# Kernel tuning notes

Measured on AMD Instinct MI355X. Metric: run time of the kernel, lower is better.

Reference implementation:

```python
import jax, jax.numpy as jnp
import numpy as np

K = 9  # kernel_size (knn neighbors, loop=True -> self included)

def setup_inputs() -> dict:
    key = jax.random.key(0)
    k1, k2, k3 = jax.random.split(key, 3)
    B, C, H, W = 8, 64, 32, 32
    OUT = 64
    x = jax.random.normal(k1, (B, C, H, W), dtype=jnp.float32)
    # SAGEConv params: lin_l (neighbor aggregate, with bias), lin_r (root, no bias)
    s = 1.0 / np.sqrt(C)
    W_l = jax.random.uniform(k2, (OUT, C), minval=-s, maxval=s, dtype=jnp.float32)
    b_l = jnp.zeros((OUT,), dtype=jnp.float32)
    W_r = jax.random.uniform(k3, (OUT, C), minval=-s, maxval=s, dtype=jnp.float32)
    return {"x": x, "W_l": W_l, "b_l": b_l, "W_r": W_r}

def _knn_mean(x_f, batches):
    # squared-euclidean pairwise distances [N, N], masked across batches
    sq = jnp.sum(x_f * x_f, axis=-1)
    dist = sq[:, None] + sq[None, :] - 2.0 * (x_f @ x_f.T)
    cross = batches[:, None] != batches[None, :]
    dist = jnp.where(cross, jnp.inf, dist)
    neg, idx = jax.lax.top_k(-dist, K)          # k nearest (self included, dist 0)
    valid = (neg != -jnp.inf).astype(x_f.dtype)  # handle degenerate last-batch node
    nbr = x_f[idx] * valid[..., None]            # [N, K, C]
    return nbr.sum(axis=1) / valid.sum(axis=1, keepdims=True)

def reference(x, W_l, b_l, W_r):
    B, C, H, Wd = x.shape
    N = B * H * Wd
    x_f = x.transpose(0, 2, 3, 1).reshape(N, C)  # flat_nodes: [B*H*W, C]
    # torch.linspace(0, B, steps=N).to(int64): truncation of i*B/(N-1)
    batches = jnp.linspace(0.0, float(B), N).astype(jnp.int32)
    mean_nbr = _knn_mean(x_f, batches)
    # SAGEConv: lin_l(mean_j x_j) + lin_r(x_i)
    return mean_nbr @ W_l.T + b_l + x_f @ W_r.T
```

## Files before the change

kernel.cpp:

```cpp
#include <hip/hip_runtime.h>
#include <cstdint>
#include <cstddef>


typedef float nf4 __attribute__((ext_vector_type(4)));

__global__ __launch_bounds__(256, 2) void k_all(const float* __restrict__ x,
                                                const float* __restrict__ Wl,
                                                const float* __restrict__ bl,
                                                const float* __restrict__ Wr,
                                                float* __restrict__ out) {
  __shared__ float R0[16384];
  __shared__ float Asf[1024];
  __shared__ float sqX[1024];
  float4* Xs4 = (float4*)R0;
  float4* As4 = (float4*)Asf;
  float4* sqX4 = (float4*)sqX;

  int bi = (int)blockIdx.x, t = threadIdx.x;
  int n0 = bi << 4;
  int s = (n0 >= 7168) ? 7168 : (n0 & ~1023);
  const float* xb = x + (((size_t)(s >> 10)) << 16);
  const float* xrow = x + (((size_t)(n0 >> 10)) << 16) + (n0 & 1023);

  {
    int c = t >> 2, r4 = t & 3;
    As4[(c << 2) + r4] = *(const float4*)&xrow[((size_t)c << 10) + (r4 << 2)];
  }

  float acc[8][8];
#pragma unroll
  for (int r = 0; r < 8; ++r)
#pragma unroll
    for (int c = 0; c < 8; ++c) acc[r][c] = 0.f;
  float4 p4 = {0.f, 0.f, 0.f, 0.f};
  int h = t >> 7, cg = t & 127;

#pragma unroll 1
  for (int ks = 0; ks < 4; ++ks) {
    if (ks) __syncthreads();
    int k0 = ks << 4;
#pragma unroll 4
    for (int i = 0; i < 16; ++i) {
      int lin = t + (i << 8);
      int kc = lin >> 8, j4 = lin & 255;
      Xs4[(kc << 8) + j4] =
          *(const float4*)&xb[((size_t)(k0 + kc) << 10) + (j4 << 2)];
    }
    __syncthreads();
#pragma unroll
    for (int kc = 0; kc < 16; ++kc) {
      float4 v = Xs4[(kc << 8) + t];
      p4.x = fmaf(v.x, v.x, p4.x);
      p4.y = fmaf(v.y, v.y, p4.y);
      p4.z = fmaf(v.z, v.z, p4.z);
      p4.w = fmaf(v.w, v.w, p4.w);
    }
#pragma unroll
    for (int kc = 0; kc < 16; ++kc) {
      float4 a0 = As4[((k0 + kc) << 2) + (h << 1)];
      float4 a1 = As4[((k0 + kc) << 2) + (h << 1) + 1];
      float4 b0 = Xs4[(kc << 8) + cg];
      float4 b1 = Xs4[(kc << 8) + 128 + cg];
      float av[8] = {a0.x, a0.y, a0.z, a0.w, a1.x, a1.y, a1.z, a1.w};
      float bv[8] = {b0.x, b0.y, b0.z, b0.w, b1.x, b1.y, b1.z, b1.w};
#pragma unroll
      for (int r = 0; r < 8; ++r)
#pragma unroll
        for (int c = 0; c < 8; ++c)
          acc[r][c] = fmaf(av[r], bv[c], acc[r][c]);
    }
  }
  sqX4[t] = p4;
  __syncthreads();

  {
    float4 sj0 = sqX4[cg];
    float4 sj1 = sqX4[128 + cg];
    int jb = (n0 - s) + (h << 3);
#pragma unroll
    for (int r = 0; r < 8; ++r) {
      float si = sqX[jb + r];
      nf4 o0 = {si + sj0.x - 2.f * acc[r][0], si + sj0.y - 2.f * acc[r][1],
                si + sj0.z - 2.f * acc[r][2], si + sj0.w - 2.f * acc[r][3]};
      nf4 o1 = {si + sj1.x - 2.f * acc[r][4], si + sj1.y - 2.f * acc[r][5],
                si + sj1.z - 2.f * acc[r][6], si + sj1.w - 2.f * acc[r][7]};
      int row = (h << 3) + r;
      *(nf4*)&R0[(row << 10) + (cg << 2)] = o0;
      *(nf4*)&R0[(row << 10) + 512 + (cg << 2)] = o1;
    }
  }
  __syncthreads();

  int lane = t & 63, w = t >> 6;
  float msum[4], xr[4];
  int cnt[4];
#pragma unroll 1
  for (int rr = 0; rr < 4; ++rr) {
    int rl = (w << 2) + rr;
    int n = n0 + rl;
    float xself = x[(((size_t)(n >> 10)) << 16) + ((size_t)lane << 10) + (n & 1023)];
    xr[rr] = xself;
    if (n == 8191) { msum[rr] = xself; cnt[rr] = 1; continue; }
    cnt[rr] = 9;
    bool mlast = (n >= 7168);
    unsigned long long cand[16];
#pragma unroll
    for (int q = 0; q < 4; ++q) {
      nf4 v = *(const nf4*)&R0[(rl << 10) + (q << 8) + (lane << 2)];
      float vv[4] = {v.x, v.y, v.z, v.w};
#pragma unroll
      for (int e = 0; e < 4; ++e) {
        unsigned u = __float_as_uint(vv[e]);
        u = (u & 0x80000000u) ? ~u : (u | 0x80000000u);
        unsigned jj = (unsigned)((q << 8) + (lane << 2) + e);
        cand[(q << 2) + e] = ((unsigned long long)u << 32) | jj;
      }
    }
    if (mlast && lane == 63) cand[15] = ~0ull;
    unsigned long long m1 = cand[0], m2 = cand[1];
    if (m2 < m1) { unsigned long long tt = m1; m1 = m2; m2 = tt; }
#pragma unroll
    for (int q = 2; q < 16; ++q) {
      unsigned long long c = cand[q];
      unsigned long long lo = (c < m1) ? c : m1;
      unsigned long long hi = (c < m1) ? m1 : c;
      m2 = (hi < m2) ? hi : m2;
      m1 = lo;
    }
    unsigned long long lm = m1;
    unsigned rmask = 0;
    bool stale = false;
    unsigned jloc[9];
#pragma unroll
    for (int kk = 0; kk < 9; ++kk) {
      unsigned long long g = lm;
#pragma unroll
      for (int off = 32; off; off >>= 1) {
        unsigned ghi = __shfl_xor((unsigned)(g >> 32), off, 64);
        unsigned glo = __shfl_xor((unsigned)g, off, 64);
        unsigned long long o = ((unsigned long long)ghi << 32) | glo;
        g = (o < g) ? o : g;
      }
      jloc[kk] = (unsigned)g & 1023u;
      if (lm == g) {
        unsigned slot = (((unsigned)g >> 6) & 12u) | ((unsigned)g & 3u);
        rmask |= 1u << slot;
        if (!stale) { lm = m2; stale = true; }
        else {
          unsigned long long best = ~0ull;
#pragma unroll
          for (int q = 0; q < 16; ++q) {
            bool alive = ((rmask >> q) & 1u) == 0u;
            unsigned long long c = cand[q];
            best = (alive && c < best) ? c : best;
          }
          lm = best;
        }
      }
    }
    const float* gx = xb + ((size_t)lane << 10);
    float g0 = gx[jloc[0]], g1 = gx[jloc[1]], g2 = gx[jloc[2]];
    float g3 = gx[jloc[3]], g4 = gx[jloc[4]], g5 = gx[jloc[5]];
    float g6 = gx[jloc[6]], g7 = gx[jloc[7]], g8 = gx[jloc[8]];
    msum[rr] = (((g0 + g1) + (g2 + g3)) + ((g4 + g5) + (g6 + g7))) + g8;
  }
  __syncthreads();

#pragma unroll 4
  for (int i = 0; i < 16; ++i) {
    int lin = t + (i << 8);
    int o = lin >> 6, c = lin & 63;
    R0[o * 65 + c] = Wl[lin];
    R0[4160 + o * 65 + c] = Wr[lin];
  }
  __syncthreads();

  float bias = bl[lane];
  float ms[4];
#pragma unroll
  for (int rr = 0; rr < 4; ++rr)
    ms[rr] = (cnt[rr] == 9) ? msum[rr] * (1.f / 9.f) : msum[rr];
  float accL[4] = {0.f, 0.f, 0.f, 0.f};
  float accR[4] = {0.f, 0.f, 0.f, 0.f};
#pragma unroll
  for (int c = 0; c < 64; ++c) {
    float wlc = R0[lane * 65 + c];
    float wrc = R0[4160 + lane * 65 + c];
#pragma unroll
    for (int rr = 0; rr < 4; ++rr) {
      float mc = __int_as_float(__builtin_amdgcn_readlane(__float_as_int(ms[rr]), c));
      float xc = __int_as_float(__builtin_amdgcn_readlane(__float_as_int(xr[rr]), c));
      accL[rr] = fmaf(mc, wlc, accL[rr]);
      accR[rr] = fmaf(xc, wrc, accR[rr]);
    }
  }
#pragma unroll
  for (int rr = 0; rr < 4; ++rr)
    __builtin_nontemporal_store(accL[rr] + accR[rr] + bias,
                                &out[((size_t)(n0 + (w << 2) + rr) << 6) + lane]);
}

extern "C" void kernel_launch(void* const* d_in, const int* in_sizes, int n_in,
                              void* d_out, int out_size, void* d_ws, size_t ws_size,
                              hipStream_t stream) {
  const float* x  = (const float*)d_in[0];
  const float* Wl = (const float*)d_in[1];
  const float* bl = (const float*)d_in[2];
  const float* Wr = (const float*)d_in[3];
  float* out = (float*)d_out;
  (void)d_ws; (void)ws_size;

  k_all<<<dim3(512), 256, 0, stream>>>(x, Wl, bl, Wr, out);
}
```

Measured before the change: 104.6 us.

## Halve rows per block and keep distance tiles in registers for top-k

Each block now handles 8 query rows instead of 16, and the grid doubles to 1024 blocks. The GEMM tile is remapped so each wave computes the distances for its own two rows across all 1024 candidates. The top-k selection then reads those distances straight from registers, so the 16x1024 distance buffer in shared memory and its extra barrier are gone. Shared memory per block drops enough to allow 4 blocks per CU. The cost is that the candidate tile of x is loaded and the squared norms are recomputed twice as often across the grid.

```diff
diff --git a/kernel.cpp b/kernel.cpp
--- a/kernel.cpp
+++ b/kernel.cpp
@@ -3,45 +3,44 @@
 #include <cstddef>
 
 
-typedef float nf4 __attribute__((ext_vector_type(4)));
-
-__global__ __launch_bounds__(256, 2) void k_all(const float* __restrict__ x,
+__global__ __launch_bounds__(256, 4) void k_all(const float* __restrict__ x,
                                                 const float* __restrict__ Wl,
                                                 const float* __restrict__ bl,
                                                 const float* __restrict__ Wr,
                                                 float* __restrict__ out) {
-  __shared__ float R0[16384];
-  __shared__ float Asf[1024];
-  __shared__ float sqX[1024];
-  float4* Xs4 = (float4*)R0;
-  float4* As4 = (float4*)Asf;
+  __shared__ float SH[9728];
+  float* Xs = SH;
+  float* Asf = SH + 8192;
+  float* sqX = SH + 8704;
+  float4* Xs4 = (float4*)Xs;
   float4* sqX4 = (float4*)sqX;
 
   int bi = (int)blockIdx.x, t = threadIdx.x;
-  int n0 = bi << 4;
+  int lane = t & 63, w = t >> 6;
+  int n0 = bi << 3;
   int s = (n0 >= 7168) ? 7168 : (n0 & ~1023);
   const float* xb = x + (((size_t)(s >> 10)) << 16);
   const float* xrow = x + (((size_t)(n0 >> 10)) << 16) + (n0 & 1023);
 
-  {
-    int c = t >> 2, r4 = t & 3;
-    As4[(c << 2) + r4] = *(const float4*)&xrow[((size_t)c << 10) + (r4 << 2)];
-  }
-
-  float acc[8][8];
-#pragma unroll
-  for (int r = 0; r < 8; ++r)
-#pragma unroll
-    for (int c = 0; c < 8; ++c) acc[r][c] = 0.f;
+  if (t < 128) {
+    int ch = t >> 1, hf = t & 1;
+    *(float4*)&Asf[(ch << 3) + (hf << 2)] =
+        *(const float4*)&xrow[((size_t)ch << 10) + (hf << 2)];
+  }
+
+  float acc[2][16];
+#pragma unroll
+  for (int r = 0; r < 2; ++r)
+#pragma unroll
+    for (int c = 0; c < 16; ++c) acc[r][c] = 0.f;
   float4 p4 = {0.f, 0.f, 0.f, 0.f};
-  int h = t >> 7, cg = t & 127;
 
 #pragma unroll 1
-  for (int ks = 0; ks < 4; ++ks) {
+  for (int ks = 0; ks < 8; ++ks) {
     if (ks) __syncthreads();
-    int k0 = ks << 4;
-#pragma unroll 4
-    for (int i = 0; i < 16; ++i) {
+    int k0 = ks << 3;
+#pragma unroll
+    for (int i = 0; i < 8; ++i) {
       int lin = t + (i << 8);
       int kc = lin >> 8, j4 = lin & 255;
       Xs4[(kc << 8) + j4] =
@@ -49,7 +48,7 @@
     }
     __syncthreads();
 #pragma unroll
-    for (int kc = 0; kc < 16; ++kc) {
+    for (int kc = 0; kc < 8; ++kc) {
       float4 v = Xs4[(kc << 8) + t];
       p4.x = fmaf(v.x, v.x, p4.x);
       p4.y = fmaf(v.y, v.y, p4.y);
@@ -57,61 +56,47 @@
       p4.w = fmaf(v.w, v.w, p4.w);
     }
 #pragma unroll
-    for (int kc = 0; kc < 16; ++kc) {
-      float4 a0 = As4[((k0 + kc) << 2) + (h << 1)];
-      float4 a1 = As4[((k0 + kc) << 2) + (h << 1) + 1];
-      float4 b0 = Xs4[(kc << 8) + cg];
-      float4 b1 = Xs4[(kc << 8) + 128 + cg];
-      float av[8] = {a0.x, a0.y, a0.z, a0.w, a1.x, a1.y, a1.z, a1.w};
-      float bv[8] = {b0.x, b0.y, b0.z, b0.w, b1.x, b1.y, b1.z, b1.w};
-#pragma unroll
-      for (int r = 0; r < 8; ++r)
-#pragma unroll
-        for (int c = 0; c < 8; ++c)
-          acc[r][c] = fmaf(av[r], bv[c], acc[r][c]);
+    for (int kc = 0; kc < 8; ++kc) {
+      float2 a = *(const float2*)&Asf[((k0 + kc) << 3) + (w << 1)];
+      float4 b0 = Xs4[(kc << 8) + lane];
+      float4 b1 = Xs4[(kc << 8) + 64 + lane];
+      float4 b2 = Xs4[(kc << 8) + 128 + lane];
+      float4 b3 = Xs4[(kc << 8) + 192 + lane];
+      float bv[16] = {b0.x, b0.y, b0.z, b0.w, b1.x, b1.y, b1.z, b1.w,
+                      b2.x, b2.y, b2.z, b2.w, b3.x, b3.y, b3.z, b3.w};
+#pragma unroll
+      for (int c = 0; c < 16; ++c) {
+        acc[0][c] = fmaf(a.x, bv[c], acc[0][c]);
+        acc[1][c] = fmaf(a.y, bv[c], acc[1][c]);
+      }
     }
   }
   sqX4[t] = p4;
   __syncthreads();
 
-  {
-    float4 sj0 = sqX4[cg];
-    float4 sj1 = sqX4[128 + cg];
-    int jb = (n0 - s) + (h << 3);
-#pragma unroll
-    for (int r = 0; r < 8; ++r) {
-      float si = sqX[jb + r];
-      nf4 o0 = {si + sj0.x - 2.f * acc[r][0], si + sj0.y - 2.f * acc[r][1],
-                si + sj0.z - 2.f * acc[r][2], si + sj0.w - 2.f * acc[r][3]};
-      nf4 o1 = {si + sj1.x - 2.f * acc[r][4], si + sj1.y - 2.f * acc[r][5],
-                si + sj1.z - 2.f * acc[r][6], si + sj1.w - 2.f * acc[r][7]};
-      int row = (h << 3) + r;
-      *(nf4*)&R0[(row << 10) + (cg << 2)] = o0;
-      *(nf4*)&R0[(row << 10) + 512 + (cg << 2)] = o1;
-    }
-  }
-  __syncthreads();
-
-  int lane = t & 63, w = t >> 6;
-  float msum[4], xr[4];
-  int cnt[4];
+  float4 sq4[4];
+#pragma unroll
+  for (int q = 0; q < 4; ++q) sq4[q] = sqX4[(q << 6) + lane];
+
+  float msum[2], xr[2];
+  int cnt[2];
 #pragma unroll 1
-  for (int rr = 0; rr < 4; ++rr) {
-    int rl = (w << 2) + rr;
-    int n = n0 + rl;
+  for (int rr = 0; rr < 2; ++rr) {
+    int n = n0 + (w << 1) + rr;
     float xself = x[(((size_t)(n >> 10)) << 16) + ((size_t)lane << 10) + (n & 1023)];
     xr[rr] = xself;
     if (n == 8191) { msum[rr] = xself; cnt[rr] = 1; continue; }
     cnt[rr] = 9;
+    float si = sqX[n - s];
     bool mlast = (n >= 7168);
     unsigned long long cand[16];
 #pragma unroll
     for (int q = 0; q < 4; ++q) {
-      nf4 v = *(const nf4*)&R0[(rl << 10) + (q << 8) + (lane << 2)];
-      float vv[4] = {v.x, v.y, v.z, v.w};
+      float sj[4] = {sq4[q].x, sq4[q].y, sq4[q].z, sq4[q].w};
 #pragma unroll
       for (int e = 0; e < 4; ++e) {
-        unsigned u = __float_as_uint(vv[e]);
+        float d = (si + sj[e]) - 2.f * acc[rr][(q << 2) + e];
+        unsigned u = __float_as_uint(d);
         u = (u & 0x80000000u) ? ~u : (u | 0x80000000u);
         unsigned jj = (unsigned)((q << 8) + (lane << 2) + e);
         cand[(q << 2) + e] = ((unsigned long long)u << 32) | jj;
@@ -167,28 +152,28 @@
   }
   __syncthreads();
 
-#pragma unroll 4
+#pragma unroll
   for (int i = 0; i < 16; ++i) {
     int lin = t + (i << 8);
     int o = lin >> 6, c = lin & 63;
-    R0[o * 65 + c] = Wl[lin];
-    R0[4160 + o * 65 + c] = Wr[lin];
+    SH[o * 65 + c] = Wl[lin];
+    SH[4160 + o * 65 + c] = Wr[lin];
   }
   __syncthreads();
 
   float bias = bl[lane];
-  float ms[4];
-#pragma unroll
-  for (int rr = 0; rr < 4; ++rr)
+  float ms[2];
+#pragma unroll
+  for (int rr = 0; rr < 2; ++rr)
     ms[rr] = (cnt[rr] == 9) ? msum[rr] * (1.f / 9.f) : msum[rr];
-  float accL[4] = {0.f, 0.f, 0.f, 0.f};
-  float accR[4] = {0.f, 0.f, 0.f, 0.f};
+  float accL[2] = {0.f, 0.f};
+  float accR[2] = {0.f, 0.f};
 #pragma unroll
   for (int c = 0; c < 64; ++c) {
-    float wlc = R0[lane * 65 + c];
-    float wrc = R0[4160 + lane * 65 + c];
-#pragma unroll
-    for (int rr = 0; rr < 4; ++rr) {
+    float wlc = SH[lane * 65 + c];
+    float wrc = SH[4160 + lane * 65 + c];
+#pragma unroll
+    for (int rr = 0; rr < 2; ++rr) {
       float mc = __int_as_float(__builtin_amdgcn_readlane(__float_as_int(ms[rr]), c));
       float xc = __int_as_float(__builtin_amdgcn_readlane(__float_as_int(xr[rr]), c));
       accL[rr] = fmaf(mc, wlc, accL[rr]);
@@ -196,9 +181,9 @@
     }
   }
 #pragma unroll
-  for (int rr = 0; rr < 4; ++rr)
+  for (int rr = 0; rr < 2; ++rr)
     __builtin_nontemporal_store(accL[rr] + accR[rr] + bias,
-                                &out[((size_t)(n0 + (w << 2) + rr) << 6) + lane]);
+                                &out[((size_t)(n0 + (w << 1) + rr) << 6) + lane]);
 }
 
 extern "C" void kernel_launch(void* const* d_in, const int* in_sizes, int n_in,
@@ -211,5 +196,5 @@
   float* out = (float*)d_out;
   (void)d_ws; (void)ws_size;
 
-  k_all<<<dim3(512), 256, 0, stream>>>(x, Wl, bl, Wr, out);
+  k_all<<<dim3(1024), 256, 0, stream>>>(x, Wl, bl, Wr, out);
 }
```

Result: slower. 137.3 us (+31.3%).
